# Optimization experiments

Measured on AMD Instinct MI355X. Metric: run time of the kernel, lower is better.

## Reference

```python
import jax, jax.numpy as jnp
import numpy as np

EPS = 1e-8
THRESHOLD_FACTOR = 0.5


def setup_inputs() -> dict:
    key = jax.random.key(0)
    k1, k2, k3 = jax.random.split(key, 3)
    B, S, D_IN, D_OUT = 4, 4096, 2048, 2048
    x = jax.random.normal(k1, (B, S, D_IN), dtype=jnp.float32)
    # kaiming-uniform-like init for weight
    bound = 1.0 / np.sqrt(D_IN)
    weight = jax.random.uniform(k2, (D_OUT, D_IN), dtype=jnp.float32,
                                minval=-np.sqrt(3.0) * bound, maxval=np.sqrt(3.0) * bound)
    row_scale = jnp.ones((D_OUT, 1), dtype=jnp.float32)
    bias = jax.random.uniform(k3, (D_OUT,), dtype=jnp.float32, minval=-bound, maxval=bound)
    g = jnp.ones((D_IN,), dtype=jnp.float32)  # input RMSNorm affine weight
    return {"x": x, "weight": weight, "row_scale": row_scale, "bias": bias, "g": g}


def _rms_norm(v, axis):
    return v * jax.lax.rsqrt(jnp.mean(v * v, axis=axis, keepdims=True) + EPS)


def reference(x, weight, row_scale, bias, g):
    # input RMSNorm with affine scale
    xn = _rms_norm(x, -1) * g  # [B,S,Din]
    # row RMSNorm of weight
    w = _rms_norm(weight, 1)  # [Dout,Din]
    # abs-mean threshold ternary quantization
    abs_mean = jnp.mean(jnp.abs(w), axis=1, keepdims=True)  # [Dout,1]
    mask = (jnp.abs(w) > THRESHOLD_FACTOR * abs_mean).astype(w.dtype)
    w_q = jnp.sign(w) * mask  # ternary {-1,0,1}
    # scaled dequant: per-row abs_mean and learned row_scale
    w_eff = w_q * abs_mean * row_scale  # [Dout,Din]
    out = jnp.einsum('bsd,od->bso', xn, w_eff) + bias
    return out
```

## Files before the change

### kernel.cpp

```cpp
#include <hip/hip_runtime.h>
#include <stdint.h>

#define EPSF 1e-8f

using i32x4 = __attribute__((ext_vector_type(4))) int;

__device__ __forceinline__ float wave_sum(float v) {
#pragma unroll
  for (int off = 32; off > 0; off >>= 1) v += __shfl_down(v, off, 64);
  return v;
}
__device__ __forceinline__ float wave_max(float v) {
#pragma unroll
  for (int off = 32; off > 0; off >>= 1) v = fmaxf(v, __shfl_down(v, off, 64));
  return v;
}

__global__ __launch_bounds__(256) void wquant_kernel(
    const float* __restrict__ w, const float* __restrict__ row_scale,
    signed char* __restrict__ wq, float* __restrict__ scale, int K) {
  const int row = blockIdx.x;
  const int t = threadIdx.x;
  const float* wr = w + (size_t)row * K;
  float4 v0 = reinterpret_cast<const float4*>(wr)[2 * t];
  float4 v1 = reinterpret_cast<const float4*>(wr)[2 * t + 1];
  float f[8] = {v0.x, v0.y, v0.z, v0.w, v1.x, v1.y, v1.z, v1.w};
  float sa = 0.f, sq = 0.f;
#pragma unroll
  for (int i = 0; i < 8; ++i) { sa += fabsf(f[i]); sq += f[i] * f[i]; }
  sa = wave_sum(sa);
  sq = wave_sum(sq);
  __shared__ float smA[4], smQ[4];
  const int wid = t >> 6;
  if ((t & 63) == 0) { smA[wid] = sa; smQ[wid] = sq; }
  __syncthreads();
  const float sumabs = smA[0] + smA[1] + smA[2] + smA[3];
  const float sumsq  = smQ[0] + smQ[1] + smQ[2] + smQ[3];
  const float absmean = sumabs / (float)K;
  const float thr = 0.5f * absmean;
  union { signed char c[8]; uint2 u; } pk;
#pragma unroll
  for (int i = 0; i < 8; ++i)
    pk.c[i] = (fabsf(f[i]) > thr) ? (f[i] > 0.f ? (signed char)1 : (signed char)-1)
                                  : (signed char)0;
  reinterpret_cast<uint2*>(wq + (size_t)row * K)[t] = pk.u;
  if (t == 0)
    scale[row] = absmean * rsqrtf(sumsq / (float)K + EPSF) * row_scale[row];
}

__global__ __launch_bounds__(256) void xnorm_kernel(
    const float* __restrict__ x, const float* __restrict__ g,
    signed char* __restrict__ xq, float* __restrict__ sx, int K) {
  const int row = blockIdx.x;
  const int t = threadIdx.x;
  const float* xr = x + (size_t)row * K;
  float4 v0 = reinterpret_cast<const float4*>(xr)[2 * t];
  float4 v1 = reinterpret_cast<const float4*>(xr)[2 * t + 1];
  float f[8] = {v0.x, v0.y, v0.z, v0.w, v1.x, v1.y, v1.z, v1.w};
  float sq = 0.f;
#pragma unroll
  for (int i = 0; i < 8; ++i) sq += f[i] * f[i];
  sq = wave_sum(sq);
  __shared__ float smQ[4], smM[4];
  const int wid = t >> 6;
  if ((t & 63) == 0) smQ[wid] = sq;
  __syncthreads();
  const float sumsq = smQ[0] + smQ[1] + smQ[2] + smQ[3];
  const float rs = rsqrtf(sumsq / (float)K + EPSF);
  float4 g0 = reinterpret_cast<const float4*>(g)[2 * t];
  float4 g1 = reinterpret_cast<const float4*>(g)[2 * t + 1];
  float gg[8] = {g0.x, g0.y, g0.z, g0.w, g1.x, g1.y, g1.z, g1.w};
  float vv[8]; float am = 0.f;
#pragma unroll
  for (int i = 0; i < 8; ++i) {
    vv[i] = f[i] * rs * gg[i];
    am = fmaxf(am, fabsf(vv[i]));
  }
  am = wave_max(am);
  if ((t & 63) == 0) smM[wid] = am;
  __syncthreads();
  const float amax = fmaxf(fmaxf(smM[0], smM[1]), fmaxf(smM[2], smM[3]));
  const float inv = amax > 0.f ? 127.f / amax : 0.f;
  union { signed char c[8]; uint2 u; } pk;
#pragma unroll
  for (int i = 0; i < 8; ++i)
    pk.c[i] = (signed char)__float2int_rn(vv[i] * inv);
  reinterpret_cast<uint2*>(xq + (size_t)row * K)[t] = pk.u;
  if (t == 0) sx[row] = amax > 0.f ? amax / 127.f : 0.f;
}


#define BAR() do { __builtin_amdgcn_sched_barrier(0); \
                   asm volatile("" ::: "memory"); \
                   __builtin_amdgcn_s_barrier(); \
                   asm volatile("" ::: "memory"); \
                   __builtin_amdgcn_sched_barrier(0); } while (0)
#define VM(n) asm volatile("s_waitcnt vmcnt(" #n ")" ::: "memory")

__global__ __launch_bounds__(512, 2) void gemm_kernel(
    const signed char* __restrict__ A,
    const signed char* __restrict__ B,
    const float* __restrict__ scale, const float* __restrict__ bias,
    const float* __restrict__ sx,
    float* __restrict__ C, int M, int N, int K) {
  __shared__ signed char lds[2][2][2][16384];

  const int tid  = threadIdx.x;
  const int lane = tid & 63;
  const int wid  = tid >> 6;
  const int wm   = wid >> 2;
  const int wn   = wid & 3;
  const int fr   = lane & 15;
  const int kq   = lane >> 4;

  const int nwg = gridDim.x;
  const int cpx = nwg >> 3;
  const int swz = (blockIdx.x & 7) * cpx + (blockIdx.x >> 3);
  const int NBN = N >> 8;
  const int bn = swz % NBN;
  const int bm = swz / NBN;
  const int mBase = bm * 256, nBase = bn * 256;

  const size_t Kb = (size_t)K;

  const int sr = tid >> 3;
  const int gsrc = (tid & 7) ^ (sr & 7);
  const char* Abyte = (const char*)A + (size_t)(mBase + sr) * Kb + gsrc * 16;
  const char* Bbyte = (const char*)B +
      (size_t)(nBase + ((sr >> 5) * 64) + (sr & 31)) * Kb + gsrc * 16;

#define STAGE_A(bufi, h, t) do { \
    __builtin_amdgcn_global_load_lds( \
      (const __attribute__((address_space(1))) void*)(Abyte + (size_t)((h) * 64) * Kb + (size_t)(t) * 128), \
      (__attribute__((address_space(3))) void*)(&lds[bufi][0][h][tid * 16]), 16, 0, 0); \
    __builtin_amdgcn_global_load_lds( \
      (const __attribute__((address_space(1))) void*)(Abyte + (size_t)(128 + (h) * 64) * Kb + (size_t)(t) * 128), \
      (__attribute__((address_space(3))) void*)(&lds[bufi][0][h][8192 + tid * 16]), 16, 0, 0); \
  } while (0)

#define STAGE_B(bufi, h, t) do { \
    __builtin_amdgcn_global_load_lds( \
      (const __attribute__((address_space(1))) void*)(Bbyte + (size_t)((h) * 32) * Kb + (size_t)(t) * 128), \
      (__attribute__((address_space(3))) void*)(&lds[bufi][1][h][tid * 16]), 16, 0, 0); \
    __builtin_amdgcn_global_load_lds( \
      (const __attribute__((address_space(1))) void*)(Bbyte + (size_t)(128 + (h) * 32) * Kb + (size_t)(t) * 128), \
      (__attribute__((address_space(3))) void*)(&lds[bufi][1][h][8192 + tid * 16]), 16, 0, 0); \
  } while (0)

  const int slot0 = ((kq ^ (fr & 7)) << 4);
  const int aRowB = (wm * 64 + fr) * 128;
  const int bRowB = (wn * 32 + fr) * 128;

  i32x4 aF[4][2], bF[4][2];
  i32x4 acc[8][4];
#pragma unroll
  for (int m = 0; m < 8; ++m)
#pragma unroll
    for (int n = 0; n < 4; ++n) acc[m][n] = (i32x4){0, 0, 0, 0};

#define LDA(bufi, mg) do { \
    _Pragma("unroll") for (int mm = 0; mm < 4; ++mm) \
    _Pragma("unroll") for (int s = 0; s < 2; ++s) \
      aF[mm][s] = *(const i32x4*)&lds[bufi][0][mg][ \
          aRowB + mm * 2048 + (slot0 ^ (s << 6))]; \
  } while (0)

#define LDB(bufi, np) do { \
    _Pragma("unroll") for (int nn = 0; nn < 2; ++nn) \
    _Pragma("unroll") for (int s = 0; s < 2; ++s) \
      bF[(np) * 2 + nn][s] = *(const i32x4*)&lds[bufi][1][np][ \
          bRowB + nn * 2048 + (slot0 ^ (s << 6))]; \
  } while (0)

#define MFMA_Q(mg, np) do { \
    __builtin_amdgcn_s_setprio(1); \
    _Pragma("unroll") for (int mm = 0; mm < 4; ++mm) \
    _Pragma("unroll") for (int nn = 0; nn < 2; ++nn) { \
      i32x4 c = acc[(mg) * 4 + mm][(np) * 2 + nn]; \
      c = __builtin_amdgcn_mfma_i32_16x16x64_i8(aF[mm][0], bF[(np) * 2 + nn][0], c, 0, 0, 0); \
      c = __builtin_amdgcn_mfma_i32_16x16x64_i8(aF[mm][1], bF[(np) * 2 + nn][1], c, 0, 0, 0); \
      acc[(mg) * 4 + mm][(np) * 2 + nn] = c; \
    } \
    __builtin_amdgcn_s_setprio(0); } while (0)

  const int crowBase = mBase + wm * 128 + kq * 4;
  const int ccolBase = nBase + wn * 64 + fr;

#define STORE_Q(mg, np) do { \
    float sxq_[4][4]; \
    _Pragma("unroll") for (int mm = 0; mm < 4; ++mm) \
    _Pragma("unroll") for (int r = 0; r < 4; ++r) \
      sxq_[mm][r] = sx[crowBase + ((mg) * 4 + mm) * 16 + r]; \
    _Pragma("unroll") for (int nn = 0; nn < 2; ++nn) { \
      const int gc = ccolBase + ((np) * 2 + nn) * 16; \
      const float sc = scale[gc]; \
      const float bi = bias[gc]; \
      _Pragma("unroll") for (int mm = 0; mm < 4; ++mm) { \
        const int r0 = crowBase + ((mg) * 4 + mm) * 16; \
        _Pragma("unroll") for (int r = 0; r < 4; ++r) \
          C[(size_t)(r0 + r) * (size_t)N + (size_t)gc] = \
              (float)acc[(mg) * 4 + mm][(np) * 2 + nn][r] * (sxq_[mm][r] * sc) + bi; \
      } } } while (0)

  STAGE_A(0, 0, 0); STAGE_B(0, 0, 0);
  STAGE_A(0, 1, 0); STAGE_B(0, 1, 0);
  STAGE_A(1, 0, 1); STAGE_B(1, 0, 1);

  const int NT = K >> 7;
  for (int i = 0; i < (NT >> 1) - 1; ++i) {
    const int t1  = 2 * i + 1;
    const int tn0 = 2 * i + 2;
    const int tn1 = 2 * i + 3;
    VM(4); BAR();
    STAGE_A(1, 1, t1); STAGE_B(1, 1, t1);
    LDA(0, 0); LDB(0, 0); LDB(0, 1);
    MFMA_Q(0, 0); MFMA_Q(0, 1);
    BAR();
    STAGE_A(0, 0, tn0); STAGE_B(0, 0, tn0);
    LDA(0, 1);
    MFMA_Q(1, 0); MFMA_Q(1, 1);
    VM(4); BAR();
    STAGE_A(0, 1, tn0); STAGE_B(0, 1, tn0);
    LDA(1, 0); LDB(1, 0); LDB(1, 1);
    MFMA_Q(0, 0); MFMA_Q(0, 1);
    BAR();
    STAGE_A(1, 0, tn1); STAGE_B(1, 0, tn1);
    LDA(1, 1);
    MFMA_Q(1, 0); MFMA_Q(1, 1);
  }

  {
    const int tl = NT - 1;
    VM(4); BAR();
    STAGE_A(1, 1, tl); STAGE_B(1, 1, tl);
    LDA(0, 0); LDB(0, 0); LDB(0, 1);
    MFMA_Q(0, 0); MFMA_Q(0, 1);
    BAR();
    LDA(0, 1);
    MFMA_Q(1, 0); MFMA_Q(1, 1);
    VM(0); BAR();
    LDA(1, 0); LDB(1, 0); LDB(1, 1);
    MFMA_Q(0, 0); STORE_Q(0, 0);
    MFMA_Q(0, 1); STORE_Q(0, 1);
    BAR();
    LDA(1, 1);
    MFMA_Q(1, 0); STORE_Q(1, 0);
    MFMA_Q(1, 1); STORE_Q(1, 1);
  }
#undef STAGE_A
#undef STAGE_B
#undef LDA
#undef LDB
#undef MFMA_Q
#undef STORE_Q
}

extern "C" void kernel_launch(void* const* d_in, const int* in_sizes, int n_in,
                              void* d_out, int out_size, void* d_ws, size_t ws_size,
                              hipStream_t stream) {
  const float* x         = (const float*)d_in[0];
  const float* weight    = (const float*)d_in[1];
  const float* row_scale = (const float*)d_in[2];
  const float* bias      = (const float*)d_in[3];
  const float* g         = (const float*)d_in[4];
  float* out = (float*)d_out;

  const int Din  = in_sizes[4];
  const int Dout = in_sizes[3];
  const int Mrows = in_sizes[0] / Din;

  char* ws = (char*)d_ws;
  signed char* wq = (signed char*)ws;
  signed char* xq = (signed char*)(ws + (size_t)Dout * Din);
  float* scale = (float*)(ws + (size_t)Dout * Din + (size_t)Mrows * Din);
  float* sx = scale + Dout;

  wquant_kernel<<<Dout, 256, 0, stream>>>(weight, row_scale, wq, scale, Din);
  xnorm_kernel<<<Mrows, 256, 0, stream>>>(x, g, xq, sx, Din);
  const int grid = (Mrows / 256) * (Dout / 256);
  gemm_kernel<<<grid, 512, 0, stream>>>(xq, wq, scale, bias, sx, out,
                                        Mrows, Dout, Din);
}
```

Measured before the change: 116.4 us.

## Merge prep kernels and retile GEMM to 256x128 with triple-buffered K=64 pipeline

The weight-quantize and activation-norm kernels are fused into a single launch, with the block index selecting which job a block does. The GEMM moves from 256x256 tiles with 512 threads and K=128 double-buffered stages to 256x128 tiles with 256 threads. It now uses a three-stage ring of K=64 LDS buffers with one barrier per iteration. Each wave still holds a 128x64 accumulator, but the grid doubles in block count and there are more, shorter K iterations. This trades per-block data reuse for better occupancy and a simpler pipeline.

```diff
diff --git a/kernel.cpp b/kernel.cpp
--- a/kernel.cpp
+++ b/kernel.cpp
@@ -16,77 +16,76 @@
   return v;
 }
 
-__global__ __launch_bounds__(256) void wquant_kernel(
+__global__ __launch_bounds__(256) void prep_kernel(
+    const float* __restrict__ x, const float* __restrict__ g,
     const float* __restrict__ w, const float* __restrict__ row_scale,
-    signed char* __restrict__ wq, float* __restrict__ scale, int K) {
-  const int row = blockIdx.x;
+    signed char* __restrict__ xq, float* __restrict__ sx,
+    signed char* __restrict__ wq, float* __restrict__ scale,
+    int K, int Dout) {
+  __shared__ float smA[4], smQ[4], smM[4];
   const int t = threadIdx.x;
-  const float* wr = w + (size_t)row * K;
-  float4 v0 = reinterpret_cast<const float4*>(wr)[2 * t];
-  float4 v1 = reinterpret_cast<const float4*>(wr)[2 * t + 1];
-  float f[8] = {v0.x, v0.y, v0.z, v0.w, v1.x, v1.y, v1.z, v1.w};
-  float sa = 0.f, sq = 0.f;
-#pragma unroll
-  for (int i = 0; i < 8; ++i) { sa += fabsf(f[i]); sq += f[i] * f[i]; }
-  sa = wave_sum(sa);
-  sq = wave_sum(sq);
-  __shared__ float smA[4], smQ[4];
   const int wid = t >> 6;
-  if ((t & 63) == 0) { smA[wid] = sa; smQ[wid] = sq; }
-  __syncthreads();
-  const float sumabs = smA[0] + smA[1] + smA[2] + smA[3];
-  const float sumsq  = smQ[0] + smQ[1] + smQ[2] + smQ[3];
-  const float absmean = sumabs / (float)K;
-  const float thr = 0.5f * absmean;
-  union { signed char c[8]; uint2 u; } pk;
-#pragma unroll
-  for (int i = 0; i < 8; ++i)
-    pk.c[i] = (fabsf(f[i]) > thr) ? (f[i] > 0.f ? (signed char)1 : (signed char)-1)
-                                  : (signed char)0;
-  reinterpret_cast<uint2*>(wq + (size_t)row * K)[t] = pk.u;
-  if (t == 0)
-    scale[row] = absmean * rsqrtf(sumsq / (float)K + EPSF) * row_scale[row];
-}
-
-__global__ __launch_bounds__(256) void xnorm_kernel(
-    const float* __restrict__ x, const float* __restrict__ g,
-    signed char* __restrict__ xq, float* __restrict__ sx, int K) {
-  const int row = blockIdx.x;
-  const int t = threadIdx.x;
-  const float* xr = x + (size_t)row * K;
-  float4 v0 = reinterpret_cast<const float4*>(xr)[2 * t];
-  float4 v1 = reinterpret_cast<const float4*>(xr)[2 * t + 1];
-  float f[8] = {v0.x, v0.y, v0.z, v0.w, v1.x, v1.y, v1.z, v1.w};
-  float sq = 0.f;
-#pragma unroll
-  for (int i = 0; i < 8; ++i) sq += f[i] * f[i];
-  sq = wave_sum(sq);
-  __shared__ float smQ[4], smM[4];
-  const int wid = t >> 6;
-  if ((t & 63) == 0) smQ[wid] = sq;
-  __syncthreads();
-  const float sumsq = smQ[0] + smQ[1] + smQ[2] + smQ[3];
-  const float rs = rsqrtf(sumsq / (float)K + EPSF);
-  float4 g0 = reinterpret_cast<const float4*>(g)[2 * t];
-  float4 g1 = reinterpret_cast<const float4*>(g)[2 * t + 1];
-  float gg[8] = {g0.x, g0.y, g0.z, g0.w, g1.x, g1.y, g1.z, g1.w};
-  float vv[8]; float am = 0.f;
-#pragma unroll
-  for (int i = 0; i < 8; ++i) {
-    vv[i] = f[i] * rs * gg[i];
-    am = fmaxf(am, fabsf(vv[i]));
-  }
-  am = wave_max(am);
-  if ((t & 63) == 0) smM[wid] = am;
-  __syncthreads();
-  const float amax = fmaxf(fmaxf(smM[0], smM[1]), fmaxf(smM[2], smM[3]));
-  const float inv = amax > 0.f ? 127.f / amax : 0.f;
-  union { signed char c[8]; uint2 u; } pk;
-#pragma unroll
-  for (int i = 0; i < 8; ++i)
-    pk.c[i] = (signed char)__float2int_rn(vv[i] * inv);
-  reinterpret_cast<uint2*>(xq + (size_t)row * K)[t] = pk.u;
-  if (t == 0) sx[row] = amax > 0.f ? amax / 127.f : 0.f;
+  if ((int)blockIdx.x < Dout) {
+    const int row = blockIdx.x;
+    const float* wr = w + (size_t)row * K;
+    float4 v0 = reinterpret_cast<const float4*>(wr)[2 * t];
+    float4 v1 = reinterpret_cast<const float4*>(wr)[2 * t + 1];
+    float f[8] = {v0.x, v0.y, v0.z, v0.w, v1.x, v1.y, v1.z, v1.w};
+    float sa = 0.f, sq = 0.f;
+#pragma unroll
+    for (int i = 0; i < 8; ++i) { sa += fabsf(f[i]); sq += f[i] * f[i]; }
+    sa = wave_sum(sa);
+    sq = wave_sum(sq);
+    if ((t & 63) == 0) { smA[wid] = sa; smQ[wid] = sq; }
+    __syncthreads();
+    const float sumabs = smA[0] + smA[1] + smA[2] + smA[3];
+    const float sumsq  = smQ[0] + smQ[1] + smQ[2] + smQ[3];
+    const float absmean = sumabs / (float)K;
+    const float thr = 0.5f * absmean;
+    union { signed char c[8]; uint2 u; } pk;
+#pragma unroll
+    for (int i = 0; i < 8; ++i)
+      pk.c[i] = (fabsf(f[i]) > thr)
+                    ? (f[i] > 0.f ? (signed char)1 : (signed char)-1)
+                    : (signed char)0;
+    reinterpret_cast<uint2*>(wq + (size_t)row * K)[t] = pk.u;
+    if (t == 0)
+      scale[row] = absmean * rsqrtf(sumsq / (float)K + EPSF) * row_scale[row];
+  } else {
+    const int row = blockIdx.x - Dout;
+    const float* xr = x + (size_t)row * K;
+    float4 v0 = reinterpret_cast<const float4*>(xr)[2 * t];
+    float4 v1 = reinterpret_cast<const float4*>(xr)[2 * t + 1];
+    float f[8] = {v0.x, v0.y, v0.z, v0.w, v1.x, v1.y, v1.z, v1.w};
+    float sq = 0.f;
+#pragma unroll
+    for (int i = 0; i < 8; ++i) sq += f[i] * f[i];
+    sq = wave_sum(sq);
+    if ((t & 63) == 0) smQ[wid] = sq;
+    __syncthreads();
+    const float sumsq = smQ[0] + smQ[1] + smQ[2] + smQ[3];
+    const float rs = rsqrtf(sumsq / (float)K + EPSF);
+    float4 g0 = reinterpret_cast<const float4*>(g)[2 * t];
+    float4 g1 = reinterpret_cast<const float4*>(g)[2 * t + 1];
+    float gg[8] = {g0.x, g0.y, g0.z, g0.w, g1.x, g1.y, g1.z, g1.w};
+    float vv[8]; float am = 0.f;
+#pragma unroll
+    for (int i = 0; i < 8; ++i) {
+      vv[i] = f[i] * rs * gg[i];
+      am = fmaxf(am, fabsf(vv[i]));
+    }
+    am = wave_max(am);
+    if ((t & 63) == 0) smM[wid] = am;
+    __syncthreads();
+    const float amax = fmaxf(fmaxf(smM[0], smM[1]), fmaxf(smM[2], smM[3]));
+    const float inv = amax > 0.f ? 127.f / amax : 0.f;
+    union { signed char c[8]; uint2 u; } pk;
+#pragma unroll
+    for (int i = 0; i < 8; ++i)
+      pk.c[i] = (signed char)__float2int_rn(vv[i] * inv);
+    reinterpret_cast<uint2*>(xq + (size_t)row * K)[t] = pk.u;
+    if (t == 0) sx[row] = amax > 0.f ? amax / 127.f : 0.f;
+  }
 }
 
 
@@ -97,162 +96,122 @@
                    __builtin_amdgcn_sched_barrier(0); } while (0)
 #define VM(n) asm volatile("s_waitcnt vmcnt(" #n ")" ::: "memory")
 
-__global__ __launch_bounds__(512, 2) void gemm_kernel(
+#define LDSBUF 24576
+
+__global__ __launch_bounds__(256, 2) void gemm_kernel(
     const signed char* __restrict__ A,
     const signed char* __restrict__ B,
     const float* __restrict__ scale, const float* __restrict__ bias,
     const float* __restrict__ sx,
     float* __restrict__ C, int M, int N, int K) {
-  __shared__ signed char lds[2][2][2][16384];
+  __shared__ signed char lds[3 * LDSBUF];
 
   const int tid  = threadIdx.x;
   const int lane = tid & 63;
   const int wid  = tid >> 6;
-  const int wm   = wid >> 2;
-  const int wn   = wid & 3;
+  const int wm   = wid >> 1;
+  const int wn   = wid & 1;
   const int fr   = lane & 15;
   const int kq   = lane >> 4;
 
   const int nwg = gridDim.x;
   const int cpx = nwg >> 3;
   const int swz = (blockIdx.x & 7) * cpx + (blockIdx.x >> 3);
-  const int NBN = N >> 8;
+  const int NBN = N >> 7;
   const int bn = swz % NBN;
   const int bm = swz / NBN;
-  const int mBase = bm * 256, nBase = bn * 256;
+  const int mBase = bm * 256, nBase = bn * 128;
 
   const size_t Kb = (size_t)K;
 
-  const int sr = tid >> 3;
-  const int gsrc = (tid & 7) ^ (sr & 7);
+  const int sr = tid >> 2;
+  const int gsrc = (tid & 3) ^ ((sr >> 1) & 3);
   const char* Abyte = (const char*)A + (size_t)(mBase + sr) * Kb + gsrc * 16;
-  const char* Bbyte = (const char*)B +
-      (size_t)(nBase + ((sr >> 5) * 64) + (sr & 31)) * Kb + gsrc * 16;
-
-#define STAGE_A(bufi, h, t) do { \
-    __builtin_amdgcn_global_load_lds( \
-      (const __attribute__((address_space(1))) void*)(Abyte + (size_t)((h) * 64) * Kb + (size_t)(t) * 128), \
-      (__attribute__((address_space(3))) void*)(&lds[bufi][0][h][tid * 16]), 16, 0, 0); \
-    __builtin_amdgcn_global_load_lds( \
-      (const __attribute__((address_space(1))) void*)(Abyte + (size_t)(128 + (h) * 64) * Kb + (size_t)(t) * 128), \
-      (__attribute__((address_space(3))) void*)(&lds[bufi][0][h][8192 + tid * 16]), 16, 0, 0); \
+  const char* Bbyte = (const char*)B + (size_t)(nBase + sr) * Kb + gsrc * 16;
+
+#define STAGE(off, t) do { \
+    _Pragma("unroll") for (int i_ = 0; i_ < 4; ++i_) \
+      __builtin_amdgcn_global_load_lds( \
+        (const __attribute__((address_space(1))) void*)(Abyte + (size_t)(64 * i_) * Kb + (size_t)(t) * 64), \
+        (__attribute__((address_space(3))) void*)(&lds[(off) + i_ * 4096 + tid * 16]), 16, 0, 0); \
+    _Pragma("unroll") for (int i_ = 0; i_ < 2; ++i_) \
+      __builtin_amdgcn_global_load_lds( \
+        (const __attribute__((address_space(1))) void*)(Bbyte + (size_t)(64 * i_) * Kb + (size_t)(t) * 64), \
+        (__attribute__((address_space(3))) void*)(&lds[(off) + 16384 + i_ * 4096 + tid * 16]), 16, 0, 0); \
   } while (0)
 
-#define STAGE_B(bufi, h, t) do { \
-    __builtin_amdgcn_global_load_lds( \
-      (const __attribute__((address_space(1))) void*)(Bbyte + (size_t)((h) * 32) * Kb + (size_t)(t) * 128), \
-      (__attribute__((address_space(3))) void*)(&lds[bufi][1][h][tid * 16]), 16, 0, 0); \
-    __builtin_amdgcn_global_load_lds( \
-      (const __attribute__((address_space(1))) void*)(Bbyte + (size_t)(128 + (h) * 32) * Kb + (size_t)(t) * 128), \
-      (__attribute__((address_space(3))) void*)(&lds[bufi][1][h][8192 + tid * 16]), 16, 0, 0); \
+  const int aSlot = ((kq ^ ((fr >> 1) & 3)) << 4);
+  const int aRowB = (wm * 128 + fr) * 64;
+  const int bRowB = 16384 + (wn * 64 + fr) * 64;
+
+  i32x4 aF[8], bF[4];
+  i32x4 acc[8][4];
+#pragma unroll
+  for (int m = 0; m < 8; ++m)
+#pragma unroll
+    for (int n = 0; n < 4; ++n) acc[m][n] = (i32x4){0, 0, 0, 0};
+
+#define READS(off) do { \
+    _Pragma("unroll") for (int mm = 0; mm < 8; ++mm) \
+      aF[mm] = *(const i32x4*)&lds[(off) + aRowB + mm * 1024 + aSlot]; \
+    _Pragma("unroll") for (int nn = 0; nn < 4; ++nn) \
+      bF[nn] = *(const i32x4*)&lds[(off) + bRowB + nn * 1024 + aSlot]; \
   } while (0)
 
-  const int slot0 = ((kq ^ (fr & 7)) << 4);
-  const int aRowB = (wm * 64 + fr) * 128;
-  const int bRowB = (wn * 32 + fr) * 128;
-
-  i32x4 aF[4][2], bF[4][2];
-  i32x4 acc[8][4];
-#pragma unroll
-  for (int m = 0; m < 8; ++m)
-#pragma unroll
-    for (int n = 0; n < 4; ++n) acc[m][n] = (i32x4){0, 0, 0, 0};
-
-#define LDA(bufi, mg) do { \
-    _Pragma("unroll") for (int mm = 0; mm < 4; ++mm) \
-    _Pragma("unroll") for (int s = 0; s < 2; ++s) \
-      aF[mm][s] = *(const i32x4*)&lds[bufi][0][mg][ \
-          aRowB + mm * 2048 + (slot0 ^ (s << 6))]; \
-  } while (0)
-
-#define LDB(bufi, np) do { \
-    _Pragma("unroll") for (int nn = 0; nn < 2; ++nn) \
-    _Pragma("unroll") for (int s = 0; s < 2; ++s) \
-      bF[(np) * 2 + nn][s] = *(const i32x4*)&lds[bufi][1][np][ \
-          bRowB + nn * 2048 + (slot0 ^ (s << 6))]; \
-  } while (0)
-
-#define MFMA_Q(mg, np) do { \
+#define MFMAS() do { \
     __builtin_amdgcn_s_setprio(1); \
-    _Pragma("unroll") for (int mm = 0; mm < 4; ++mm) \
-    _Pragma("unroll") for (int nn = 0; nn < 2; ++nn) { \
-      i32x4 c = acc[(mg) * 4 + mm][(np) * 2 + nn]; \
-      c = __builtin_amdgcn_mfma_i32_16x16x64_i8(aF[mm][0], bF[(np) * 2 + nn][0], c, 0, 0, 0); \
-      c = __builtin_amdgcn_mfma_i32_16x16x64_i8(aF[mm][1], bF[(np) * 2 + nn][1], c, 0, 0, 0); \
-      acc[(mg) * 4 + mm][(np) * 2 + nn] = c; \
-    } \
+    _Pragma("unroll") for (int mm = 0; mm < 8; ++mm) \
+    _Pragma("unroll") for (int nn = 0; nn < 4; ++nn) \
+      acc[mm][nn] = __builtin_amdgcn_mfma_i32_16x16x64_i8( \
+          aF[mm], bF[nn], acc[mm][nn], 0, 0, 0); \
     __builtin_amdgcn_s_setprio(0); } while (0)
+
+  STAGE(0, 0);
+  STAGE(LDSBUF, 1);
+  unsigned int oRd = 0, oMid = LDSBUF, oWr = 2 * LDSBUF;
+
+  const int NT = K >> 6;
+  for (int t = 0; t < NT - 2; ++t) {
+    VM(6); BAR();
+    STAGE(oWr, t + 2);
+    READS(oRd);
+    MFMAS();
+    const unsigned int tmp = oRd; oRd = oMid; oMid = oWr; oWr = tmp;
+  }
+  VM(6); BAR();
+  READS(oRd);
+  MFMAS();
+  { const unsigned int tmp = oRd; oRd = oMid; oMid = oWr; oWr = tmp; }
+  VM(0); BAR();
+  READS(oRd);
+  MFMAS();
 
   const int crowBase = mBase + wm * 128 + kq * 4;
   const int ccolBase = nBase + wn * 64 + fr;
-
-#define STORE_Q(mg, np) do { \
-    float sxq_[4][4]; \
-    _Pragma("unroll") for (int mm = 0; mm < 4; ++mm) \
-    _Pragma("unroll") for (int r = 0; r < 4; ++r) \
-      sxq_[mm][r] = sx[crowBase + ((mg) * 4 + mm) * 16 + r]; \
-    _Pragma("unroll") for (int nn = 0; nn < 2; ++nn) { \
-      const int gc = ccolBase + ((np) * 2 + nn) * 16; \
-      const float sc = scale[gc]; \
-      const float bi = bias[gc]; \
-      _Pragma("unroll") for (int mm = 0; mm < 4; ++mm) { \
-        const int r0 = crowBase + ((mg) * 4 + mm) * 16; \
-        _Pragma("unroll") for (int r = 0; r < 4; ++r) \
-          C[(size_t)(r0 + r) * (size_t)N + (size_t)gc] = \
-              (float)acc[(mg) * 4 + mm][(np) * 2 + nn][r] * (sxq_[mm][r] * sc) + bi; \
-      } } } while (0)
-
-  STAGE_A(0, 0, 0); STAGE_B(0, 0, 0);
-  STAGE_A(0, 1, 0); STAGE_B(0, 1, 0);
-  STAGE_A(1, 0, 1); STAGE_B(1, 0, 1);
-
-  const int NT = K >> 7;
-  for (int i = 0; i < (NT >> 1) - 1; ++i) {
-    const int t1  = 2 * i + 1;
-    const int tn0 = 2 * i + 2;
-    const int tn1 = 2 * i + 3;
-    VM(4); BAR();
-    STAGE_A(1, 1, t1); STAGE_B(1, 1, t1);
-    LDA(0, 0); LDB(0, 0); LDB(0, 1);
-    MFMA_Q(0, 0); MFMA_Q(0, 1);
-    BAR();
-    STAGE_A(0, 0, tn0); STAGE_B(0, 0, tn0);
-    LDA(0, 1);
-    MFMA_Q(1, 0); MFMA_Q(1, 1);
-    VM(4); BAR();
-    STAGE_A(0, 1, tn0); STAGE_B(0, 1, tn0);
-    LDA(1, 0); LDB(1, 0); LDB(1, 1);
-    MFMA_Q(0, 0); MFMA_Q(0, 1);
-    BAR();
-    STAGE_A(1, 0, tn1); STAGE_B(1, 0, tn1);
-    LDA(1, 1);
-    MFMA_Q(1, 0); MFMA_Q(1, 1);
-  }
-
-  {
-    const int tl = NT - 1;
-    VM(4); BAR();
-    STAGE_A(1, 1, tl); STAGE_B(1, 1, tl);
-    LDA(0, 0); LDB(0, 0); LDB(0, 1);
-    MFMA_Q(0, 0); MFMA_Q(0, 1);
-    BAR();
-    LDA(0, 1);
-    MFMA_Q(1, 0); MFMA_Q(1, 1);
-    VM(0); BAR();
-    LDA(1, 0); LDB(1, 0); LDB(1, 1);
-    MFMA_Q(0, 0); STORE_Q(0, 0);
-    MFMA_Q(0, 1); STORE_Q(0, 1);
-    BAR();
-    LDA(1, 1);
-    MFMA_Q(1, 0); STORE_Q(1, 0);
-    MFMA_Q(1, 1); STORE_Q(1, 1);
-  }
-#undef STAGE_A
-#undef STAGE_B
-#undef LDA
-#undef LDB
-#undef MFMA_Q
-#undef STORE_Q
+  float sc[4], bi[4];
+#pragma unroll
+  for (int nn = 0; nn < 4; ++nn) {
+    sc[nn] = scale[ccolBase + nn * 16];
+    bi[nn] = bias[ccolBase + nn * 16];
+  }
+#pragma unroll
+  for (int mm = 0; mm < 8; ++mm) {
+    const int r0 = crowBase + mm * 16;
+    float sxv[4];
+#pragma unroll
+    for (int r = 0; r < 4; ++r) sxv[r] = sx[r0 + r];
+#pragma unroll
+    for (int nn = 0; nn < 4; ++nn) {
+      const int gc = ccolBase + nn * 16;
+#pragma unroll
+      for (int r = 0; r < 4; ++r)
+        C[(size_t)(r0 + r) * (size_t)N + (size_t)gc] =
+            (float)acc[mm][nn][r] * (sxv[r] * sc[nn]) + bi[nn];
+    }
+  }
+#undef STAGE
+#undef READS
+#undef MFMAS
 }
 
 extern "C" void kernel_launch(void* const* d_in, const int* in_sizes, int n_in,
@@ -275,9 +234,9 @@
   float* scale = (float*)(ws + (size_t)Dout * Din + (size_t)Mrows * Din);
   float* sx = scale + Dout;
 
-  wquant_kernel<<<Dout, 256, 0, stream>>>(weight, row_scale, wq, scale, Din);
-  xnorm_kernel<<<Mrows, 256, 0, stream>>>(x, g, xq, sx, Din);
-  const int grid = (Mrows / 256) * (Dout / 256);
-  gemm_kernel<<<grid, 512, 0, stream>>>(xq, wq, scale, bias, sx, out,
+  prep_kernel<<<Dout + Mrows, 256, 0, stream>>>(x, g, weight, row_scale,
+                                                xq, sx, wq, scale, Din, Dout);
+  const int grid = (Mrows / 256) * (Dout / 128);
+  gemm_kernel<<<grid, 256, 0, stream>>>(xq, wq, scale, bias, sx, out,
                                         Mrows, Dout, Din);
 }
```

Result: no change. 118.3 us (+1.6%).
